# Performance work log

Hardware: AMD Instinct MI355X
Metric: run time of the kernel (lower is better)

## Reference

```python
import jax, jax.numpy as jnp
import numpy as np

N_CLI, N_AGG, E, D, L = 100000, 1000, 1600000, 128, 3


def setup_inputs() -> dict:
    key = jax.random.key(0)
    ks = jax.random.split(key, 16)
    inp = {
        'x_clients': jax.random.normal(ks[0], (N_CLI, D), jnp.float32),
        'x_agg': jax.random.normal(ks[1], (N_AGG, D), jnp.float32),
        'c2a_src': jax.random.randint(ks[2], (E,), 0, N_CLI, jnp.int32),
        'c2a_dst': jax.random.randint(ks[3], (E,), 0, N_AGG, jnp.int32),
        'a2c_src': jax.random.randint(ks[4], (E,), 0, N_AGG, jnp.int32),
        'a2c_dst': jax.random.randint(ks[5], (E,), 0, N_CLI, jnp.int32),
    }
    s = 1.0 / np.sqrt(D)
    # stacked per-layer SAGE params for each edge type: W_l (on aggregated msg), W_r (on dst), b
    inp['Wl_c2a'] = jax.random.uniform(ks[6], (L, D, D), jnp.float32, -s, s)
    inp['Wr_c2a'] = jax.random.uniform(ks[7], (L, D, D), jnp.float32, -s, s)
    inp['b_c2a'] = jax.random.uniform(ks[8], (L, D), jnp.float32, -s, s)
    inp['Wl_a2c'] = jax.random.uniform(ks[9], (L, D, D), jnp.float32, -s, s)
    inp['Wr_a2c'] = jax.random.uniform(ks[10], (L, D, D), jnp.float32, -s, s)
    inp['b_a2c'] = jax.random.uniform(ks[11], (L, D), jnp.float32, -s, s)
    inp['W_lin'] = jax.random.uniform(ks[12], (D, 1), jnp.float32, -s, s)
    inp['b_lin'] = jax.random.uniform(ks[13], (1,), jnp.float32, -s, s)
    return inp


def _sage(x_src, x_dst, src, dst, Wl, Wr, b, n_dst):
    # mean aggregation of gathered source features onto dst nodes
    msg = x_src[src]                                        # [E, D]
    summed = jax.ops.segment_sum(msg, dst, num_segments=n_dst)
    cnt = jax.ops.segment_sum(jnp.ones((src.shape[0], 1), x_src.dtype), dst, num_segments=n_dst)
    mean = summed / jnp.maximum(cnt, 1.0)
    return mean @ Wl + x_dst @ Wr + b


def _leaky(x):
    return jnp.where(x >= 0, x, 0.1 * x)


def reference(x_clients, x_agg, c2a_src, c2a_dst, a2c_src, a2c_dst,
              Wl_c2a, Wr_c2a, b_c2a, Wl_a2c, Wr_a2c, b_a2c, W_lin, b_lin):
    xc, xa = x_clients, x_agg
    for l in range(L):
        new_a = _sage(xc, xa, c2a_src, c2a_dst, Wl_c2a[l], Wr_c2a[l], b_c2a[l], N_AGG)
        new_c = _sage(xa, xc, a2c_src, a2c_dst, Wl_a2c[l], Wr_a2c[l], b_a2c[l], N_CLI)
        xa, xc = _leaky(new_a), _leaky(new_c)
    return (xc @ W_lin + b_lin).squeeze(1)
```

## Files before the change

kernel.cpp:

```cpp
#include <hip/hip_runtime.h>

#define D      128
#define NCLI   100000
#define NAGG   1000
#define NLAYER 3
#define NBKT   782
#define NRNG   8
#define NBIN   (NAGG * NRNG)
#define RMAGIC 343598u
#define NHIST  512
#define NCVTX  (NCLI * D / 4 / 256)
#define NCVTW  ((NLAYER * D * D + 255) / 256)
#define NROWT  (NCLI / 32)

typedef short bf16x8 __attribute__((ext_vector_type(8)));
typedef float f32x16 __attribute__((ext_vector_type(16)));

static __device__ __forceinline__ float leaky(float x) { return x >= 0.f ? x : 0.1f * x; }

static __device__ __forceinline__ unsigned bf16_rn(float f) {
    unsigned u = __float_as_uint(f);
    return (u + 0x7fffu + ((u >> 16) & 1u)) >> 16;
}
static __device__ __forceinline__ float bf_val(unsigned h) { return __uint_as_float(h << 16); }
static __device__ __forceinline__ unsigned pack_bf2(float lo, float hi) {
    return bf16_rn(lo) | (bf16_rn(hi) << 16);
}
static __device__ __forceinline__ float bf_lo(unsigned v) { return __uint_as_float(v << 16); }
static __device__ __forceinline__ float bf_hi(unsigned v) { return __uint_as_float(v & 0xffff0000u); }

__global__ __launch_bounds__(256) void prep(const int* __restrict__ c2a_src,
                                            const int* __restrict__ c2a_dst,
                                            const int* __restrict__ a2c_dst, int E,
                                            int* __restrict__ cnt_ar, int* __restrict__ bcnt,
                                            const float4* __restrict__ X4,
                                            uint2* __restrict__ xhi, uint2* __restrict__ xlo,
                                            const float* __restrict__ W,
                                            unsigned short* __restrict__ Wt) {
    __shared__ int h[NBIN + NBKT];
    int bid = blockIdx.x;
    if (bid < NHIST) {
        for (int i = threadIdx.x; i < NBIN + NBKT; i += 256) h[i] = 0;
        __syncthreads();
        int stride = NHIST * 256;
        for (int e = bid * 256 + threadIdx.x; e < E; e += stride) {
            int s = c2a_src[e];
            int bin = c2a_dst[e] * NRNG + (int)__umulhi((unsigned)s, RMAGIC);
            atomicAdd(&h[bin], 1);
            atomicAdd(&h[NBIN + (a2c_dst[e] >> 7)], 1);
        }
        __syncthreads();
        for (int i = threadIdx.x; i < NBIN; i += 256)
            if (h[i]) atomicAdd(&cnt_ar[i], h[i]);
        for (int i = threadIdx.x; i < NBKT; i += 256)
            if (h[NBIN + i]) atomicAdd(&bcnt[i], h[NBIN + i]);
    } else if (bid < NHIST + NCVTX) {
        int t = (bid - NHIST) * 256 + threadIdx.x;
        float4 f = X4[t];
        unsigned h0 = bf16_rn(f.x), h1 = bf16_rn(f.y), h2 = bf16_rn(f.z), h3 = bf16_rn(f.w);
        xhi[t] = make_uint2(h0 | (h1 << 16), h2 | (h3 << 16));
        xlo[t] = make_uint2(pack_bf2(f.x - bf_val(h0), f.y - bf_val(h1)),
                            pack_bf2(f.z - bf_val(h2), f.w - bf_val(h3)));
    } else {
        int idx = (bid - NHIST - NCVTX) * 256 + threadIdx.x;
        if (idx >= NLAYER * D * D) return;
        int layer = idx >> 14, rem = idx & (D * D - 1);
        int k = rem >> 7, n = rem & 127;
        float w = W[layer * D * D + k * D + n];
        unsigned hh = bf16_rn(w);
        unsigned short* base = Wt + layer * 2 * D * D;
        base[n * D + k] = (unsigned short)hh;
        base[D * D + n * D + k] = (unsigned short)bf16_rn(w - bf_val(hh));
    }
}

__global__ void scan_both(const int* __restrict__ cnt_ar, int* __restrict__ rp_ar,
                          int* __restrict__ cur_ar, const int* __restrict__ bcnt,
                          int* __restrict__ brp, int* __restrict__ bcur) {
    __shared__ int sh[1024];
    int t = threadIdx.x;
    if (blockIdx.x == 0) {
        int v[8];
        int s = 0;
#pragma unroll
        for (int j = 0; j < 8; j++) {
            int idx = t * 8 + j;
            v[j] = (idx < NBIN) ? cnt_ar[idx] : 0;
            s += v[j];
        }
        sh[t] = s;
        __syncthreads();
        for (int off = 1; off < 1024; off <<= 1) {
            int x = (t >= off) ? sh[t - off] : 0;
            __syncthreads();
            sh[t] += x;
            __syncthreads();
        }
        int run = sh[t] - s;
#pragma unroll
        for (int j = 0; j < 8; j++) {
            int idx = t * 8 + j;
            if (idx < NBIN) {
                rp_ar[idx] = run;
                cur_ar[idx] = run;
            }
            run += v[j];
        }
        if (t == 1023) rp_ar[NBIN] = sh[1023];
    } else {
        int v = (t < NBKT) ? bcnt[t] : 0;
        sh[t] = v;
        __syncthreads();
        for (int off = 1; off < 1024; off <<= 1) {
            int x = (t >= off) ? sh[t - off] : 0;
            __syncthreads();
            sh[t] += x;
            __syncthreads();
        }
        if (t == 0) { brp[0] = 0; bcur[0] = 0; }
        if (t < NBKT) {
            brp[t + 1] = sh[t];
            if (t + 1 < NBKT) bcur[t + 1] = sh[t];
        }
    }
}

__global__ __launch_bounds__(1024) void scatter_both(const int* __restrict__ c2a_src,
                                                     const int* __restrict__ c2a_dst,
                                                     const int* __restrict__ a2c_src,
                                                     const int* __restrict__ a2c_dst, int E,
                                                     int* __restrict__ cur_ar,
                                                     int* __restrict__ col_c2a,
                                                     int* __restrict__ bcur,
                                                     int* __restrict__ sorted1) {
    __shared__ int sbuf[2 * NBIN];
    int tid = threadIdx.x;
    if (blockIdx.x < 256) {
        int* h = sbuf;
        int* base = sbuf + NBIN;
        int chunk = (E + 255) / 256;
        int e0 = blockIdx.x * chunk;
        int e1 = min(E, e0 + chunk);
        for (int i = tid; i < NBIN; i += 1024) h[i] = 0;
        __syncthreads();
        for (int e = e0 + tid; e < e1; e += 1024) {
            int s = c2a_src[e];
            atomicAdd(&h[c2a_dst[e] * NRNG + (int)__umulhi((unsigned)s, RMAGIC)], 1);
        }
        __syncthreads();
        for (int i = tid; i < NBIN; i += 1024) {
            int c = h[i];
            base[i] = c ? atomicAdd(&cur_ar[i], c) : 0;
        }
        __syncthreads();
        for (int e = e0 + tid; e < e1; e += 1024) {
            int s = c2a_src[e];
            int bin = c2a_dst[e] * NRNG + (int)__umulhi((unsigned)s, RMAGIC);
            int pos = atomicAdd(&base[bin], 1);
            col_c2a[pos] = s;
        }
    } else {
        int* h = sbuf;
        int* base = sbuf + NBKT;
        int bid = blockIdx.x - 256;
        int chunk = (E + 255) / 256;
        int e0 = bid * chunk;
        int e1 = min(E, e0 + chunk);
        for (int i = tid; i < NBKT; i += 1024) h[i] = 0;
        __syncthreads();
        for (int e = e0 + tid; e < e1; e += 1024) atomicAdd(&h[a2c_dst[e] >> 7], 1);
        __syncthreads();
        for (int i = tid; i < NBKT; i += 1024) {
            int c = h[i];
            base[i] = c ? atomicAdd(&bcur[i], c) : 0;
        }
        __syncthreads();
        for (int e = e0 + tid; e < e1; e += 1024) {
            int d = a2c_dst[e];
            int pos = atomicAdd(&base[d >> 7], 1);
            sorted1[pos] = ((d & 127) << 10) | a2c_src[e];
        }
    }
}

__global__ __launch_bounds__(512) void bucket_csr(const int* __restrict__ brp,
                                                  const int* __restrict__ sorted1,
                                                  int* __restrict__ rp_c,
                                                  int* __restrict__ col) {
    __shared__ int h[128], cur[128];
    int b = blockIdx.x, tid = threadIdx.x;
    if (tid < 128) h[tid] = 0;
    __syncthreads();
    int beg = brp[b], end = brp[b + 1];
    for (int e = beg + tid; e < end; e += 512) atomicAdd(&h[sorted1[e] >> 10], 1);
    __syncthreads();
    if (tid < 128) cur[tid] = h[tid];
    __syncthreads();
    for (int off = 1; off < 128; off <<= 1) {
        int x = 0;
        if (tid < 128 && tid >= off) x = cur[tid - off];
        __syncthreads();
        if (tid < 128) cur[tid] += x;
        __syncthreads();
    }
    if (tid < 128) {
        int start = beg + cur[tid] - h[tid];
        int c = b * 128 + tid;
        if (c < NCLI) rp_c[c] = start;
        cur[tid] = start;
    }
    if (b == NBKT - 1 && tid == 0) rp_c[NCLI] = end;
    __syncthreads();
    for (int e = beg + tid; e < end; e += 512) {
        int p = sorted1[e];
        int pos = atomicAdd(&cur[p >> 10], 1);
        col[pos] = p & 1023;
    }
}


__global__ __launch_bounds__(512) void gather_mean(const unsigned* __restrict__ tbl,
                                                   const int* __restrict__ rp_ar,
                                                   const int* __restrict__ col,
                                                   float* __restrict__ psum) {
    __shared__ float part[4][8][D];
    int quad = blockIdx.x >> 3, r = blockIdx.x & 7;
    int tid = threadIdx.x;
    int a = tid >> 7;
    int sub = (tid >> 4) & 7;
    int sl = tid & 15;
    const uint4* tbl4 = (const uint4*)tbl;
    int agg = quad * 4 + a;
    int bin = agg * NRNG + r;
    int beg = rp_ar[bin], end = rp_ar[bin + 1];
    float f0 = 0, f1 = 0, f2 = 0, f3 = 0, f4 = 0, f5 = 0, f6 = 0, f7 = 0;
    int e = beg + sub;
    for (; e + 8 < end; e += 16) {
        int s0 = col[e];
        int s1 = col[e + 8];
        uint4 v0 = tbl4[(s0 << 4) + sl];
        uint4 v1 = tbl4[(s1 << 4) + sl];
        f0 += bf_lo(v0.x); f1 += bf_hi(v0.x); f2 += bf_lo(v0.y); f3 += bf_hi(v0.y);
        f4 += bf_lo(v0.z); f5 += bf_hi(v0.z); f6 += bf_lo(v0.w); f7 += bf_hi(v0.w);
        f0 += bf_lo(v1.x); f1 += bf_hi(v1.x); f2 += bf_lo(v1.y); f3 += bf_hi(v1.y);
        f4 += bf_lo(v1.z); f5 += bf_hi(v1.z); f6 += bf_lo(v1.w); f7 += bf_hi(v1.w);
    }
    if (e < end) {
        int s0 = col[e];
        uint4 v0 = tbl4[(s0 << 4) + sl];
        f0 += bf_lo(v0.x); f1 += bf_hi(v0.x); f2 += bf_lo(v0.y); f3 += bf_hi(v0.y);
        f4 += bf_lo(v0.z); f5 += bf_hi(v0.z); f6 += bf_lo(v0.w); f7 += bf_hi(v0.w);
    }
    float* pr = &part[a][sub][sl * 8];
    pr[0] = f0; pr[1] = f1; pr[2] = f2; pr[3] = f3;
    pr[4] = f4; pr[5] = f5; pr[6] = f6; pr[7] = f7;
    __syncthreads();
    int c = tid & 127;
    float s = 0.f;
#pragma unroll
    for (int g = 0; g < 8; g++) s += part[a][g][c];
    psum[((size_t)agg * NRNG + r) * D + c] = s;
}

__global__ __launch_bounds__(128) void combine_agg(const float* __restrict__ psum,
                                                   const int* __restrict__ rp_ar,
                                                   const float* xa_old,
                                                   const float* __restrict__ Wl_a2c,
                                                   const float* __restrict__ Wl_c2a,
                                                   const float* __restrict__ Wr_c2a,
                                                   const float* __restrict__ b_c2a,
                                                   unsigned short* __restrict__ ya_bf,
                                                   float* xa_out) {
    __shared__ float mr[D], xr[D];
    int i = blockIdx.x, j = threadIdx.x;
    const float* pr = psum + (size_t)i * NRNG * D + j;
    float s = 0.f;
#pragma unroll
    for (int r = 0; r < NRNG; r++) s += pr[r * D];
    int deg = rp_ar[i * NRNG + NRNG] - rp_ar[i * NRNG];
    mr[j] = s / fmaxf((float)deg, 1.f);
    xr[j] = xa_old[i * D + j];
    __syncthreads();
    float accy = 0.f, accn = b_c2a[j];
#pragma unroll 4
    for (int k = 0; k < D; k++) {
        accy += xr[k] * Wl_a2c[k * D + j];
        accn += mr[k] * Wl_c2a[k * D + j] + xr[k] * Wr_c2a[k * D + j];
    }
    ya_bf[i * D + j] = (unsigned short)bf16_rn(accy);
    xa_out[i * D + j] = leaky(accn);
}

template <int LAST>
__global__ __launch_bounds__(256) void gemm_agg(const unsigned short* __restrict__ Ahi,
                                                const unsigned short* __restrict__ Alo,
                                                const unsigned short* __restrict__ Wt,
                                                const float* __restrict__ bias,
                                                const unsigned* __restrict__ ya,
                                                const int* __restrict__ rowptr,
                                                const int* __restrict__ col,
                                                unsigned* __restrict__ xhi,
                                                unsigned* __restrict__ xlo,
                                                const float* __restrict__ Wlin,
                                                const float* __restrict__ blin,
                                                float* __restrict__ out, int E) {
    __shared__ float smem[32][D];
    int tid = threadIdx.x;
    int wave = tid >> 6, lane = tid & 63;
    int cl = lane & 31, kh = lane >> 5;
    int n0 = wave * 32;
    const unsigned short* Wlo_ = Wt + D * D;
    const unsigned short* wbh = Wt + (size_t)(n0 + cl) * D + kh * 8;
    const unsigned short* wbl = Wlo_ + (size_t)(n0 + cl) * D + kh * 8;
    bf16x8 bhi[8], blo[8];
#pragma unroll
    for (int kc = 0; kc < 8; kc++) {
        bhi[kc] = *(const bf16x8*)(wbh + kc * 16);
        blo[kc] = *(const bf16x8*)(wbl + kc * 16);
    }
    float bv = bias[n0 + cl];
    int l = lane;
    int m0 = blockIdx.x * 32;
    {
        const unsigned short* ar = Ahi + (size_t)(m0 + cl) * D + kh * 8;
        const unsigned short* al = Alo + (size_t)(m0 + cl) * D + kh * 8;
        bf16x8 ahi[8], alo[8];
#pragma unroll
        for (int kc = 0; kc < 8; kc++) {
            ahi[kc] = *(const bf16x8*)(ar + kc * 16);
            alo[kc] = *(const bf16x8*)(al + kc * 16);
        }
        f32x16 acc;
#pragma unroll
        for (int q = 0; q < 16; q++) acc[q] = bv;
#pragma unroll
        for (int kc = 0; kc < 8; kc++) {
            acc = __builtin_amdgcn_mfma_f32_32x32x16_bf16(ahi[kc], bhi[kc], acc, 0, 0, 0);
            acc = __builtin_amdgcn_mfma_f32_32x32x16_bf16(alo[kc], bhi[kc], acc, 0, 0, 0);
            acc = __builtin_amdgcn_mfma_f32_32x32x16_bf16(ahi[kc], blo[kc], acc, 0, 0, 0);
        }
#pragma unroll
        for (int reg = 0; reg < 16; reg++) {
            int row = (reg & 3) + 8 * (reg >> 2) + 4 * kh;
            smem[row][n0 + cl] = acc[reg];
        }
        __syncthreads();
        for (int i = 0; i < 8; i++) {
            int c_local = wave * 8 + i;
            int gid = m0 + c_local;
            int beg = rowptr[gid], end = rowptr[gid + 1];
            float a0 = 0, b0 = 0, a1 = 0, b1 = 0, a2 = 0, b2 = 0, a3 = 0, b3 = 0;
            float a4 = 0, b4 = 0, a5 = 0, b5 = 0, a6 = 0, b6 = 0, a7 = 0, b7 = 0;
            for (int ch = beg; ch < end; ch += 64) {
                int len = min(64, end - ch);
                int ec = col[min(ch + l, E - 1)];
                int j = 0;
                for (; j + 8 <= len; j += 8) {
                    int r0 = __shfl(ec, j + 0), r1 = __shfl(ec, j + 1);
                    int r2 = __shfl(ec, j + 2), r3 = __shfl(ec, j + 3);
                    int r4 = __shfl(ec, j + 4), r5 = __shfl(ec, j + 5);
                    int r6 = __shfl(ec, j + 6), r7 = __shfl(ec, j + 7);
                    unsigned v0 = ya[(r0 << 6) + l];
                    unsigned v1 = ya[(r1 << 6) + l];
                    unsigned v2 = ya[(r2 << 6) + l];
                    unsigned v3 = ya[(r3 << 6) + l];
                    unsigned v4 = ya[(r4 << 6) + l];
                    unsigned v5 = ya[(r5 << 6) + l];
                    unsigned v6 = ya[(r6 << 6) + l];
                    unsigned v7 = ya[(r7 << 6) + l];
                    a0 += bf_lo(v0); b0 += bf_hi(v0);
                    a1 += bf_lo(v1); b1 += bf_hi(v1);
                    a2 += bf_lo(v2); b2 += bf_hi(v2);
                    a3 += bf_lo(v3); b3 += bf_hi(v3);
                    a4 += bf_lo(v4); b4 += bf_hi(v4);
                    a5 += bf_lo(v5); b5 += bf_hi(v5);
                    a6 += bf_lo(v6); b6 += bf_hi(v6);
                    a7 += bf_lo(v7); b7 += bf_hi(v7);
                }
                for (; j < len; j++) {
                    int rr = __shfl(ec, j);
                    unsigned v = ya[(rr << 6) + l];
                    a0 += bf_lo(v); b0 += bf_hi(v);
                }
            }
            float sx = ((a0 + a1) + (a2 + a3)) + ((a4 + a5) + (a6 + a7));
            float sy = ((b0 + b1) + (b2 + b3)) + ((b4 + b5) + (b6 + b7));
            float inv = 1.f / fmaxf((float)(end - beg), 1.f);
            float2 yv = *(const float2*)&smem[c_local][2 * l];
            float r0 = leaky(yv.x + sx * inv);
            float r1 = leaky(yv.y + sy * inv);
            if (LAST) {
                float2 w = *(const float2*)&Wlin[2 * l];
                float v = r0 * w.x + r1 * w.y;
#pragma unroll
                for (int off = 32; off > 0; off >>= 1) v += __shfl_down(v, off);
                if (l == 0) out[gid] = v + blin[0];
            } else {
                unsigned h0 = bf16_rn(r0), h1 = bf16_rn(r1);
                xhi[(gid << 6) + l] = h0 | (h1 << 16);
                xlo[(gid << 6) + l] = pack_bf2(r0 - bf_val(h0), r1 - bf_val(h1));
            }
        }
    }
}

extern "C" void kernel_launch(void* const* d_in, const int* in_sizes, int n_in,
                              void* d_out, int out_size, void* d_ws, size_t ws_size,
                              hipStream_t stream) {
    const float* x_clients = (const float*)d_in[0];
    const float* x_agg     = (const float*)d_in[1];
    const int*   c2a_src   = (const int*)d_in[2];
    const int*   c2a_dst   = (const int*)d_in[3];
    const int*   a2c_src   = (const int*)d_in[4];
    const int*   a2c_dst   = (const int*)d_in[5];
    const float* Wl_c2a    = (const float*)d_in[6];
    const float* Wr_c2a    = (const float*)d_in[7];
    const float* b_c2a     = (const float*)d_in[8];
    const float* Wl_a2c    = (const float*)d_in[9];
    const float* Wr_a2c    = (const float*)d_in[10];
    const float* b_a2c     = (const float*)d_in[11];
    const float* W_lin     = (const float*)d_in[12];
    const float* b_lin     = (const float*)d_in[13];
    float* out = (float*)d_out;
    const int E = in_sizes[2];

    char* p = (char*)d_ws;
    auto alloc = [&](size_t bytes) {
        char* r = p;
        p += (bytes + 255) & ~(size_t)255;
        return r;
    };
    float*    Yb    = (float*)alloc(sizeof(float) * NCLI * D);
    unsigned* xc_hi = (unsigned*)alloc(sizeof(unsigned) * NCLI * 64);
    unsigned* xc_lo = (unsigned*)alloc(sizeof(unsigned) * NCLI * 64);
    float*    xa    = (float*)alloc(sizeof(float) * NAGG * D);
    unsigned short* ya_bf = (unsigned short*)alloc(sizeof(unsigned short) * NAGG * D);
    unsigned short* Wt = (unsigned short*)alloc(sizeof(unsigned short) * NLAYER * 2 * D * D);
    float* psum  = (float*)alloc(sizeof(float) * NAGG * NRNG * D);
    int* cnt_ar = (int*)alloc(sizeof(int) * (NBIN + NBKT));
    int* bcnt  = cnt_ar + NBIN;
    int* rp_ar = (int*)alloc(sizeof(int) * (NBIN + 1));
    int* cur_ar = (int*)alloc(sizeof(int) * NBIN);
    int* brp   = (int*)alloc(sizeof(int) * (NBKT + 1));
    int* bcur  = (int*)alloc(sizeof(int) * NBKT);
    int* rp_c  = (int*)alloc(sizeof(int) * (NCLI + 1));
    int* col_c2a = (int*)alloc(sizeof(int) * E);
    int* col_a2c = (int*)alloc(sizeof(int) * E);
    int* sorted1 = (int*)Yb;

    hipMemsetAsync(cnt_ar, 0, sizeof(int) * (NBIN + NBKT), stream);

    prep<<<NHIST + NCVTX + NCVTW, 256, 0, stream>>>(c2a_src, c2a_dst, a2c_dst, E, cnt_ar, bcnt,
                                                    (const float4*)x_clients,
                                                    (uint2*)xc_hi, (uint2*)xc_lo,
                                                    Wr_a2c, Wt);
    scan_both<<<2, 1024, 0, stream>>>(cnt_ar, rp_ar, cur_ar, bcnt, brp, bcur);
    scatter_both<<<512, 1024, 0, stream>>>(c2a_src, c2a_dst, a2c_src, a2c_dst, E,
                                           cur_ar, col_c2a, bcur, sorted1);
    bucket_csr<<<NBKT, 512, 0, stream>>>(brp, sorted1, rp_c, col_a2c);

    const float* xa_old = x_agg;
    for (int l = 0; l < NLAYER; l++) {
        gather_mean<<<(NAGG / 4) * NRNG, 512, 0, stream>>>(xc_hi, rp_ar, col_c2a, psum);
        combine_agg<<<NAGG, 128, 0, stream>>>(psum, rp_ar, xa_old,
                                              Wl_a2c + l * D * D, Wl_c2a + l * D * D,
                                              Wr_c2a + l * D * D, b_c2a + l * D, ya_bf, xa);
        if (l < NLAYER - 1) {
            gemm_agg<0><<<NROWT, 256, 0, stream>>>(
                (const unsigned short*)xc_hi, (const unsigned short*)xc_lo,
                Wt + l * 2 * D * D, b_a2c + l * D, (const unsigned*)ya_bf, rp_c, col_a2c,
                xc_hi, xc_lo, nullptr, nullptr, nullptr, E);
        } else {
            gemm_agg<1><<<NROWT, 256, 0, stream>>>(
                (const unsigned short*)xc_hi, (const unsigned short*)xc_lo,
                Wt + l * 2 * D * D, b_a2c + l * D, (const unsigned*)ya_bf, rp_c, col_a2c,
                nullptr, nullptr, W_lin, b_lin, out, E);
        }
        xa_old = xa;
    }
}
```

Baseline: 643.6 us.

## Stage block edge list in LDS and double-buffer flattened gather across wave rows

gemm_agg now loads each block's column indices into shared memory up front. It streams each wave's 8 rows as one flattened edge range, using double-buffered 16-edge gather batches, which keeps more loads in flight and removes per-row loop tails. Weight fragments are loaded inside the MFMA loop rather than preloaded into registers, which lowers register pressure. In exchange the accumulation is serialized through per-edge boundary checks, the LDS footprint grows, and there is a fallback to global col reads when a block exceeds the capacity.

```diff
diff --git a/kernel.cpp b/kernel.cpp
--- a/kernel.cpp
+++ b/kernel.cpp
@@ -12,6 +12,7 @@
 #define NCVTX  (NCLI * D / 4 / 256)
 #define NCVTW  ((NLAYER * D * D + 255) / 256)
 #define NROWT  (NCLI / 32)
+#define CAP_E  1536
 
 typedef short bf16x8 __attribute__((ext_vector_type(8)));
 typedef float f32x16 __attribute__((ext_vector_type(16)));
@@ -305,102 +306,117 @@
                                                 const float* __restrict__ blin,
                                                 float* __restrict__ out, int E) {
     __shared__ float smem[32][D];
+    __shared__ int lcol[CAP_E];
+    __shared__ int lrp[33];
     int tid = threadIdx.x;
     int wave = tid >> 6, lane = tid & 63;
     int cl = lane & 31, kh = lane >> 5;
     int n0 = wave * 32;
-    const unsigned short* Wlo_ = Wt + D * D;
-    const unsigned short* wbh = Wt + (size_t)(n0 + cl) * D + kh * 8;
-    const unsigned short* wbl = Wlo_ + (size_t)(n0 + cl) * D + kh * 8;
-    bf16x8 bhi[8], blo[8];
-#pragma unroll
-    for (int kc = 0; kc < 8; kc++) {
-        bhi[kc] = *(const bf16x8*)(wbh + kc * 16);
-        blo[kc] = *(const bf16x8*)(wbl + kc * 16);
-    }
+    int m0 = blockIdx.x * 32;
+    int blkBeg = rowptr[m0], blkEnd = rowptr[m0 + 32];
+    int nE = blkEnd - blkBeg;
+    bool inlds = (nE <= CAP_E);
+    int pv[6];
+#pragma unroll
+    for (int k = 0; k < 6; k++) pv[k] = col[min(blkBeg + tid + k * 256, E - 1)];
+    if (tid < 33) lrp[tid] = rowptr[m0 + tid];
     float bv = bias[n0 + cl];
-    int l = lane;
-    int m0 = blockIdx.x * 32;
+    f32x16 acc1;
+#pragma unroll
+    for (int qq = 0; qq < 16; qq++) acc1[qq] = bv;
     {
+        const unsigned short* Wlo_ = Wt + D * D;
         const unsigned short* ar = Ahi + (size_t)(m0 + cl) * D + kh * 8;
         const unsigned short* al = Alo + (size_t)(m0 + cl) * D + kh * 8;
-        bf16x8 ahi[8], alo[8];
+        const unsigned short* wh = Wt + (size_t)(n0 + cl) * D + kh * 8;
+        const unsigned short* wl = Wlo_ + (size_t)(n0 + cl) * D + kh * 8;
+        if (inlds) {
+#pragma unroll
+            for (int k = 0; k < 6; k++) lcol[tid + k * 256] = pv[k];
+        }
 #pragma unroll
         for (int kc = 0; kc < 8; kc++) {
-            ahi[kc] = *(const bf16x8*)(ar + kc * 16);
-            alo[kc] = *(const bf16x8*)(al + kc * 16);
-        }
-        f32x16 acc;
-#pragma unroll
-        for (int q = 0; q < 16; q++) acc[q] = bv;
-#pragma unroll
-        for (int kc = 0; kc < 8; kc++) {
-            acc = __builtin_amdgcn_mfma_f32_32x32x16_bf16(ahi[kc], bhi[kc], acc, 0, 0, 0);
-            acc = __builtin_amdgcn_mfma_f32_32x32x16_bf16(alo[kc], bhi[kc], acc, 0, 0, 0);
-            acc = __builtin_amdgcn_mfma_f32_32x32x16_bf16(ahi[kc], blo[kc], acc, 0, 0, 0);
-        }
-#pragma unroll
-        for (int reg = 0; reg < 16; reg++) {
-            int row = (reg & 3) + 8 * (reg >> 2) + 4 * kh;
-            smem[row][n0 + cl] = acc[reg];
-        }
-        __syncthreads();
-        for (int i = 0; i < 8; i++) {
-            int c_local = wave * 8 + i;
-            int gid = m0 + c_local;
-            int beg = rowptr[gid], end = rowptr[gid + 1];
-            float a0 = 0, b0 = 0, a1 = 0, b1 = 0, a2 = 0, b2 = 0, a3 = 0, b3 = 0;
-            float a4 = 0, b4 = 0, a5 = 0, b5 = 0, a6 = 0, b6 = 0, a7 = 0, b7 = 0;
-            for (int ch = beg; ch < end; ch += 64) {
-                int len = min(64, end - ch);
-                int ec = col[min(ch + l, E - 1)];
-                int j = 0;
-                for (; j + 8 <= len; j += 8) {
-                    int r0 = __shfl(ec, j + 0), r1 = __shfl(ec, j + 1);
-                    int r2 = __shfl(ec, j + 2), r3 = __shfl(ec, j + 3);
-                    int r4 = __shfl(ec, j + 4), r5 = __shfl(ec, j + 5);
-                    int r6 = __shfl(ec, j + 6), r7 = __shfl(ec, j + 7);
-                    unsigned v0 = ya[(r0 << 6) + l];
-                    unsigned v1 = ya[(r1 << 6) + l];
-                    unsigned v2 = ya[(r2 << 6) + l];
-                    unsigned v3 = ya[(r3 << 6) + l];
-                    unsigned v4 = ya[(r4 << 6) + l];
-                    unsigned v5 = ya[(r5 << 6) + l];
-                    unsigned v6 = ya[(r6 << 6) + l];
-                    unsigned v7 = ya[(r7 << 6) + l];
-                    a0 += bf_lo(v0); b0 += bf_hi(v0);
-                    a1 += bf_lo(v1); b1 += bf_hi(v1);
-                    a2 += bf_lo(v2); b2 += bf_hi(v2);
-                    a3 += bf_lo(v3); b3 += bf_hi(v3);
-                    a4 += bf_lo(v4); b4 += bf_hi(v4);
-                    a5 += bf_lo(v5); b5 += bf_hi(v5);
-                    a6 += bf_lo(v6); b6 += bf_hi(v6);
-                    a7 += bf_lo(v7); b7 += bf_hi(v7);
+            bf16x8 ahi = *(const bf16x8*)(ar + kc * 16);
+            bf16x8 alo = *(const bf16x8*)(al + kc * 16);
+            bf16x8 bh = *(const bf16x8*)(wh + kc * 16);
+            bf16x8 bl = *(const bf16x8*)(wl + kc * 16);
+            acc1 = __builtin_amdgcn_mfma_f32_32x32x16_bf16(ahi, bh, acc1, 0, 0, 0);
+            acc1 = __builtin_amdgcn_mfma_f32_32x32x16_bf16(alo, bh, acc1, 0, 0, 0);
+            acc1 = __builtin_amdgcn_mfma_f32_32x32x16_bf16(ahi, bl, acc1, 0, 0, 0);
+        }
+    }
+#pragma unroll
+    for (int reg = 0; reg < 16; reg++) {
+        int row = (reg & 3) + 8 * (reg >> 2) + 4 * kh;
+        smem[row][n0 + cl] = acc1[reg];
+    }
+    __syncthreads();
+    const int w8 = wave * 8;
+    int e0 = lrp[w8], eend = lrp[w8 + 8];
+    int cli = 0;
+    int nb = lrp[w8 + 1];
+    float s0 = 0.f, s1 = 0.f;
+    float wl0 = 0.f, wl1 = 0.f;
+    if (LAST) { float2 wv = *(const float2*)&Wlin[2 * lane]; wl0 = wv.x; wl1 = wv.y; }
+    auto flushc = [&]() {
+        int c_local = w8 + cli;
+        int gid = m0 + c_local;
+        int deg = lrp[c_local + 1] - lrp[c_local];
+        float inv = 1.f / fmaxf((float)deg, 1.f);
+        float2 yv = *(const float2*)&smem[c_local][2 * lane];
+        float r0 = leaky(yv.x + s0 * inv);
+        float r1 = leaky(yv.y + s1 * inv);
+        if (LAST) {
+            float v = r0 * wl0 + r1 * wl1;
+#pragma unroll
+            for (int off = 32; off > 0; off >>= 1) v += __shfl_down(v, off);
+            if (lane == 0) out[gid] = v + blin[0];
+        } else {
+            unsigned h0 = bf16_rn(r0), h1 = bf16_rn(r1);
+            xhi[(gid << 6) + lane] = h0 | (h1 << 16);
+            xlo[(gid << 6) + lane] = pack_bf2(r0 - bf_val(h0), r1 - bf_val(h1));
+        }
+        s0 = 0.f;
+        s1 = 0.f;
+    };
+    unsigned va[16], vb[16];
+    auto loadch = [&](unsigned (&buf)[16], int base) {
+        int pos = min(base + (lane & 15), eend - 1);
+        int ecs = inlds ? lcol[pos - blkBeg] : col[pos];
+#pragma unroll
+        for (int j = 0; j < 16; j++) {
+            int ec = __shfl(ecs, j);
+            buf[j] = ya[(ec << 6) + lane];
+        }
+    };
+    auto consume = [&](unsigned (&buf)[16], int ck) {
+#pragma unroll
+        for (int j = 0; j < 16; j++) {
+            if (ck + j < eend) {
+                while (ck + j == nb) {
+                    flushc();
+                    cli++;
+                    nb = lrp[w8 + cli + 1];
                 }
-                for (; j < len; j++) {
-                    int rr = __shfl(ec, j);
-                    unsigned v = ya[(rr << 6) + l];
-                    a0 += bf_lo(v); b0 += bf_hi(v);
-                }
+                s0 += bf_lo(buf[j]);
+                s1 += bf_hi(buf[j]);
             }
-            float sx = ((a0 + a1) + (a2 + a3)) + ((a4 + a5) + (a6 + a7));
-            float sy = ((b0 + b1) + (b2 + b3)) + ((b4 + b5) + (b6 + b7));
-            float inv = 1.f / fmaxf((float)(end - beg), 1.f);
-            float2 yv = *(const float2*)&smem[c_local][2 * l];
-            float r0 = leaky(yv.x + sx * inv);
-            float r1 = leaky(yv.y + sy * inv);
-            if (LAST) {
-                float2 w = *(const float2*)&Wlin[2 * l];
-                float v = r0 * w.x + r1 * w.y;
-#pragma unroll
-                for (int off = 32; off > 0; off >>= 1) v += __shfl_down(v, off);
-                if (l == 0) out[gid] = v + blin[0];
-            } else {
-                unsigned h0 = bf16_rn(r0), h1 = bf16_rn(r1);
-                xhi[(gid << 6) + l] = h0 | (h1 << 16);
-                xlo[(gid << 6) + l] = pack_bf2(r0 - bf_val(h0), r1 - bf_val(h1));
+        }
+    };
+    if (e0 < eend) {
+        loadch(va, e0);
+        for (int ck = e0; ck < eend; ck += 32) {
+            if (ck + 16 < eend) loadch(vb, ck + 16);
+            consume(va, ck);
+            if (ck + 16 < eend) {
+                if (ck + 32 < eend) loadch(va, ck + 32);
+                consume(vb, ck + 16);
             }
         }
+    }
+    while (cli < 8) {
+        flushc();
+        cli++;
     }
 }
 
```

After: 650.0 us. Within noise of the previous version (+1.0%).
